# Performance work log

Hardware: AMD Instinct MI355X
Metric: run time of the kernel (lower is better)

## Reference

```python
import jax, jax.numpy as jnp
import numpy as np

B, S, E, H = 2, 2048, 1024, 16
D = E // H  # head_dim
SCALE = 1.0 / np.sqrt(D)


def rope_tables(seq_len, dim, dtype=jnp.float32):
    # matches RotaryEmbedding: inv_freq over even indices, emb = cat([freqs, freqs])
    inv_freq = 1.0 / (10000.0 ** (jnp.arange(0, dim, 2, dtype=dtype) / dim))
    t = jnp.arange(seq_len, dtype=dtype)
    freqs = t[:, None] * inv_freq[None, :]          # [S, D/2]
    emb = jnp.concatenate([freqs, freqs], axis=-1)  # [S, D]
    return jnp.cos(emb)[None, None], jnp.sin(emb)[None, None]  # [1,1,S,D]


def apply_rope(x, cos, sin):
    # x: [B,H,S,D]; interleaved rotate exactly as the torch code:
    # x2 = stack([-x[...,1::2], x[...,0::2]], -1).reshape_as(x)
    x2 = jnp.stack([-x[..., 1::2], x[..., 0::2]], axis=-1).reshape(x.shape)
    return x * cos + x2 * sin


def setup_inputs() -> dict:
    key = jax.random.key(0)
    ks = jax.random.split(key, 12)
    std = 1.0 / np.sqrt(E)
    inp = {
        "query": jax.random.normal(ks[0], (B, S, E), jnp.float32),
        "key": jax.random.normal(ks[1], (B, S, E), jnp.float32),
        "value": jax.random.normal(ks[2], (B, S, E), jnp.float32),
        "mask": jnp.ones((B, S), jnp.int32),
        "Wq": jax.random.normal(ks[3], (E, E), jnp.float32) * std,
        "bq": jax.random.normal(ks[4], (E,), jnp.float32) * std,
        "Wk": jax.random.normal(ks[5], (E, E), jnp.float32) * std,
        "bk": jax.random.normal(ks[6], (E,), jnp.float32) * std,
        "Wv": jax.random.normal(ks[7], (E, E), jnp.float32) * std,
        "bv": jax.random.normal(ks[8], (E,), jnp.float32) * std,
        "Wo": jax.random.normal(ks[9], (E, E), jnp.float32) * std,
        "bo": jax.random.normal(ks[10], (E,), jnp.float32) * std,
    }
    return inp


def reference(query, key, value, mask, Wq, bq, Wk, bk, Wv, bv, Wo, bo):
    b, sq, _ = query.shape
    sk = key.shape[1]
    # linear projections (torch Linear: x @ W.T + b), split into heads [B,H,S,D]
    Q = (query @ Wq.T + bq).reshape(b, sq, H, D).transpose(0, 2, 1, 3)
    K = (key @ Wk.T + bk).reshape(b, sk, H, D).transpose(0, 2, 1, 3)
    V = (value @ Wv.T + bv).reshape(b, sk, H, D).transpose(0, 2, 1, 3)
    cos_q, sin_q = rope_tables(sq, D)
    cos_k, sin_k = rope_tables(sk, D)
    Q = apply_rope(Q, cos_q, sin_q)
    K = apply_rope(K, cos_k, sin_k)
    scores = jnp.einsum("bhqd,bhkd->bhqk", Q, K) * SCALE
    neg_inf = jnp.finfo(scores.dtype).min
    scores = jnp.where(mask[:, None, None, :] == 0, neg_inf, scores)
    attn = jax.nn.softmax(scores, axis=-1)
    # dropout omitted (deterministic reference / eval mode)
    out = jnp.einsum("bhqk,bhkd->bhqd", attn, V)
    out = out.transpose(0, 2, 1, 3).reshape(b, sq, E)
    return out @ Wo.T + bo
```

## Files before the change

### kernel.cpp

```cpp
#include <hip/hip_runtime.h>
#include <stdint.h>

typedef unsigned short u16;
typedef __bf16 bf16x8 __attribute__((ext_vector_type(8)));
typedef float f32x4 __attribute__((ext_vector_type(4)));
typedef float f32x2 __attribute__((ext_vector_type(2)));
typedef u16 u16x4v __attribute__((ext_vector_type(4)));

#define DI __device__ __forceinline__

constexpr int BB = 2, SS = 2048, EE = 1024, HH = 16, DD = 64;
constexpr int MROWS = BB * SS;
constexpr int KDIM = 1024, NDIM = 1024;

constexpr float FM = 12.0f;
constexpr float MNEG = -30000.f;

DI u16 f2bf(float f) {
  uint32_t u = __float_as_uint(f);
  return (u16)((u + 0x7FFFu + ((u >> 16) & 1u)) >> 16);
}
DI float bf2f(u16 h) { return __uint_as_float(((uint32_t)h) << 16); }

DI uint32_t cvtpk_bf16(float a, float b) {
  uint32_t r;
  asm("v_cvt_pk_bf16_f32 %0, %1, %2" : "=v"(r) : "v"(a), "v"(b));
  return r;
}

DI void cp16(const void* g, void* lds) {
  __builtin_amdgcn_global_load_lds((const __attribute__((address_space(1))) void*)g,
                                   (__attribute__((address_space(3))) void*)lds, 16, 0, 0);
}

DI f32x4 mfma16(bf16x8 a, bf16x8 b, f32x4 c) {
  return __builtin_amdgcn_mfma_f32_16x16x32_bf16(a, b, c, 0, 0, 0);
}

__global__ __launch_bounds__(256) void prep_cast(
    const float* __restrict__ q, const float* __restrict__ k, const float* __restrict__ v,
    const float* __restrict__ wq, const float* __restrict__ wk, const float* __restrict__ wv,
    const float* __restrict__ wo,
    u16* __restrict__ qb, u16* __restrict__ kb, u16* __restrict__ vb,
    u16* __restrict__ wqb, u16* __restrict__ wkb, u16* __restrict__ wvb,
    u16* __restrict__ wob) {
  constexpr size_t SZI = (size_t)MROWS * EE;
  constexpr size_t SZW = (size_t)EE * EE;
  const size_t g = ((size_t)blockIdx.x * 256 + threadIdx.x) * 4;
  const float* src; u16* dst; size_t o;
  if (g < SZI)          { src = q; dst = qb; o = g; }
  else if (g < 2 * SZI) { src = k; dst = kb; o = g - SZI; }
  else if (g < 3 * SZI) { src = v; dst = vb; o = g - 2 * SZI; }
  else {
    size_t t2 = g - 3 * SZI;
    int wi = (int)(t2 / SZW);
    o = t2 - (size_t)(wi < 4 ? wi : 3) * SZW;
    src = wi == 0 ? wq : wi == 1 ? wk : wi == 2 ? wv : wo;
    dst = wi == 0 ? wqb : wi == 1 ? wkb : wi == 2 ? wvb : wob;
  }
  const float4 f = *(const float4*)(src + o);
  u16x4v hv;
  hv[0] = f2bf(f.x); hv[1] = f2bf(f.y); hv[2] = f2bf(f.z); hv[3] = f2bf(f.w);
  *(u16x4v*)(dst + o) = hv;
}

__global__ __launch_bounds__(256) void rope_tables_k(float* __restrict__ csT,
                                                     const int* __restrict__ mask,
                                                     float* __restrict__ mfl) {
  const int t = blockIdx.x * 256 + threadIdx.x;
  const int s = t >> 6, d = t & 63, j = d & 31;
  const float ang = (float)s * exp2f(-(float)j * 0.4152410118f);
  float2 cs; cs.x = cosf(ang); cs.y = sinf(ang);
  ((float2*)csT)[t] = cs;
  if (t < BB * SS) mfl[t] = mask[t] ? -FM : MNEG;
}

__global__ __launch_bounds__(256) void gemm_qkv(
    const u16* __restrict__ qb, const u16* __restrict__ kb, const u16* __restrict__ vb,
    const u16* __restrict__ wqb, const u16* __restrict__ wkb, const u16* __restrict__ wvb,
    const float* __restrict__ bq, const float* __restrict__ bk, const float* __restrict__ bv,
    u16* __restrict__ Qp, u16* __restrict__ Kp, u16* __restrict__ Vtg,
    const float* __restrict__ csT) {
  __shared__ alignas(16) u16 sA[2][128 * 64];
  __shared__ alignas(16) u16 sB[2][128 * 64];
  const int tsel = blockIdx.y >> 5;
  const bool vtr = (tsel == 2);
  const u16* A    = tsel == 0 ? wqb : tsel == 1 ? wkb : vb;
  const u16* Bm   = tsel == 0 ? qb  : tsel == 1 ? kb  : wvb;
  const float* bias = tsel == 0 ? bq : tsel == 1 ? bk : bv;

  const int fBase = blockIdx.x * 128;
  const int tBase = (blockIdx.y & 31) * 128;
  const int aBase = vtr ? tBase : fBase;
  const int bBase = vtr ? fBase : tBase;
  const int tid = threadIdx.x;
  const int lane = tid & 63, w = tid >> 6;
  const int quad = lane >> 4, l16 = lane & 15;
  const int wr = w >> 1, wc = w & 1;

  size_t aSrc[4], bSrc[4];
  int dOff[4];
#pragma unroll
  for (int j = 0; j < 4; ++j) {
    const int c = tid + j * 256;
    const int row = c >> 3, sl = c & 7;
    const size_t off = (size_t)row * KDIM + ((sl ^ (row & 7)) * 8);
    aSrc[j] = (size_t)aBase * KDIM + off;
    bSrc[j] = (size_t)bBase * KDIM + off;
    dOff[j] = c * 8;
  }

  f32x4 acc[4][4];
#pragma unroll
  for (int mi = 0; mi < 4; ++mi)
#pragma unroll
    for (int ni = 0; ni < 4; ++ni)
#pragma unroll
      for (int e = 0; e < 4; ++e) acc[mi][ni][e] = 0.f;

  const int arow = wr * 64 + l16, brow = wc * 64 + l16;

  auto stage = [&](int k0, int bi) {
#pragma unroll
    for (int j = 0; j < 4; ++j) {
      cp16(A + aSrc[j] + k0, &sA[bi][dOff[j]]);
      cp16(Bm + bSrc[j] + k0, &sB[bi][dOff[j]]);
    }
  };

  stage(0, 0);
  __syncthreads();
  int buf = 0;
  for (int k0 = 0; k0 < KDIM; k0 += 64) {
    if (k0 + 64 < KDIM) stage(k0 + 64, buf ^ 1);
    __builtin_amdgcn_s_setprio(1);
#pragma unroll
    for (int h = 0; h < 2; ++h) {
      bf16x8 af[4], bf[4];
#pragma unroll
      for (int i = 0; i < 4; ++i) {
        const int ar = arow + i * 16, br = brow + i * 16;
        af[i] = *(const bf16x8*)&sA[buf][ar * 64 + (((h * 4 + quad) ^ (ar & 7)) << 3)];
        bf[i] = *(const bf16x8*)&sB[buf][br * 64 + (((h * 4 + quad) ^ (br & 7)) << 3)];
      }
#pragma unroll
      for (int mi = 0; mi < 4; ++mi)
#pragma unroll
        for (int ni = 0; ni < 4; ++ni)
          acc[mi][ni] = mfma16(af[mi], bf[ni], acc[mi][ni]);
    }
    __builtin_amdgcn_s_setprio(0);
    __syncthreads();
    buf ^= 1;
  }

  if (!vtr) {
    u16* C = tsel == 0 ? Qp : Kp;
#pragma unroll
    for (int mi = 0; mi < 4; ++mi) {
      const int fm = fBase + wr * 64 + mi * 16 + quad * 4;
      const float4 b4 = *(const float4*)&bias[fm];
      const int d0 = fm & 63;
#pragma unroll
      for (int ni = 0; ni < 4; ++ni) {
        const int t = tBase + wc * 64 + ni * 16 + l16;
        const int srow = t & (SS - 1);
        const float* cs = &csT[(size_t)((srow << 6) + d0) * 2];
        const float4 cs01 = *(const float4*)cs;
        const float4 cs23 = *(const float4*)(cs + 4);
        const float v0 = acc[mi][ni][0] + b4.x;
        const float v1 = acc[mi][ni][1] + b4.y;
        const float v2 = acc[mi][ni][2] + b4.z;
        const float v3 = acc[mi][ni][3] + b4.w;
        const float o0 = v0 * cs01.x - v1 * cs01.y;
        const float o1 = v1 * cs01.z + v0 * cs01.w;
        const float o2 = v2 * cs23.x - v3 * cs23.y;
        const float o3 = v3 * cs23.z + v2 * cs23.w;
        uint2 pk;
        pk.x = cvtpk_bf16(o0, o1);
        pk.y = cvtpk_bf16(o2, o3);
        *(uint2*)&C[(size_t)t * NDIM + fm] = pk;
      }
    }
  } else {
#pragma unroll
    for (int ni = 0; ni < 4; ++ni) {
      const int f = fBase + wc * 64 + ni * 16 + l16;
      const int h = f >> 6, d = f & 63;
      const float bb = bias[f];
#pragma unroll
      for (int mi = 0; mi < 4; ++mi) {
        const int t0 = tBase + wr * 64 + mi * 16 + quad * 4;
        const int b = t0 >> 11, s0 = t0 & (SS - 1);
        const int sp0 = (s0 & ~31) | (((s0 >> 2) & 3) << 3) | (((s0 >> 4) & 1) << 2);
        uint2 pk;
        pk.x = cvtpk_bf16(acc[mi][ni][0] + bb, acc[mi][ni][1] + bb);
        pk.y = cvtpk_bf16(acc[mi][ni][2] + bb, acc[mi][ni][3] + bb);
        *(uint2*)&Vtg[((size_t)((b * 16 + h) * 64 + d)) * SS + sp0] = pk;
      }
    }
  }
}

__global__ __launch_bounds__(256, 2) void attn_kernel(
    const u16* __restrict__ Qp, const u16* __restrict__ Kp, const u16* __restrict__ Vtg,
    const float* __restrict__ mfl, u16* __restrict__ Oh) {
  __shared__ alignas(16) u16 sK[2][128 * 64];
  __shared__ alignas(16) u16 sVt[2][64 * 128];
  __shared__ alignas(16) float sMaskAll[SS];
  const int tid = threadIdx.x, lane = tid & 63, w = tid >> 6;
  const int quad = lane >> 4, l16 = lane & 15;
  const int bh = blockIdx.y, b = bh >> 4, h = bh & 15;
  const int q0 = blockIdx.x * 128 + w * 32;
  const u16* Qb = Qp + (size_t)b * SS * EE + h * DD;
  const u16* Kb = Kp + (size_t)b * SS * EE + h * DD;
  const u16* Vb = Vtg + (size_t)bh * DD * SS;
  constexpr float C1 = 0.18033688011112042f;

  bf16x8 qf[2][2];
#pragma unroll
  for (int qi = 0; qi < 2; ++qi)
#pragma unroll
    for (int ks = 0; ks < 2; ++ks)
      qf[qi][ks] = *(const bf16x8*)(Qb + (size_t)(q0 + qi * 16 + l16) * EE + ks * 32 + quad * 8);

  f32x4 oacc[2][4];
#pragma unroll
  for (int qi = 0; qi < 2; ++qi)
#pragma unroll
    for (int nd = 0; nd < 4; ++nd)
#pragma unroll
      for (int e = 0; e < 4; ++e) oacc[qi][nd][e] = 0.f;
  f32x2 sum2[2];
  sum2[0] = {0.f, 0.f}; sum2[1] = {0.f, 0.f};

  auto stage = [&](int kt, int bi) {
    const int key0 = kt * 128;
#pragma unroll
    for (int i = 0; i < 4; ++i) {
      const int c = i * 256 + tid;
      const int key = c >> 3;
      const int g8 = ((c & 7) ^ (key & 7)) * 8;
      cp16(Kb + (size_t)(key0 + key) * EE + g8, &sK[bi][c * 8]);
    }
#pragma unroll
    for (int i = 0; i < 4; ++i) {
      const int L = i * 256 + tid;
      const int d = L >> 4;
      const int g8 = ((L & 15) ^ (d & 15)) * 8;
      cp16(Vb + (size_t)d * SS + key0 + g8, &sVt[bi][L * 8]);
    }
  };

  auto compute = [&](int kt, int bi) {
    const int key0 = kt * 128;
    f32x4 sacc[2][8];
#pragma unroll
    for (int qi = 0; qi < 2; ++qi)
#pragma unroll
      for (int ni = 0; ni < 8; ++ni)
#pragma unroll
        for (int e = 0; e < 4; ++e) sacc[qi][ni][e] = 0.f;
    __builtin_amdgcn_s_setprio(1);
#pragma unroll
    for (int ks = 0; ks < 2; ++ks)
#pragma unroll
      for (int ni = 0; ni < 8; ++ni) {
        const int row = ni * 16 + l16;
        const bf16x8 kf = *(const bf16x8*)&sK[bi][row * 64 + (((ks * 4 + quad) ^ (l16 & 7)) << 3)];
#pragma unroll
        for (int qi = 0; qi < 2; ++qi)
          sacc[qi][ni] = mfma16(kf, qf[qi][ks], sacc[qi][ni]);
      }
    __builtin_amdgcn_s_setprio(0);

    uint32_t pw32[2][4][4];
#pragma unroll
    for (int qi = 0; qi < 2; ++qi)
#pragma unroll
      for (int ni = 0; ni < 8; ++ni) {
        const int kb4 = key0 + ni * 16 + quad * 4;
        const f32x2 m01 = *(const f32x2*)&sMaskAll[kb4];
        const f32x2 m23 = *(const f32x2*)&sMaskAll[kb4 + 2];
        f32x2 t01, t23;
        t01.x = sacc[qi][ni][0]; t01.y = sacc[qi][ni][1];
        t23.x = sacc[qi][ni][2]; t23.y = sacc[qi][ni][3];
        t01 = t01 * C1 + m01;
        t23 = t23 * C1 + m23;
        f32x2 p01, p23;
        p01.x = __builtin_amdgcn_exp2f(t01.x); p01.y = __builtin_amdgcn_exp2f(t01.y);
        p23.x = __builtin_amdgcn_exp2f(t23.x); p23.y = __builtin_amdgcn_exp2f(t23.y);
        sum2[qi] += p01;
        sum2[qi] += p23;
        const int k2 = ni >> 1, j2 = (ni & 1) * 2;
        pw32[qi][k2][j2]     = cvtpk_bf16(p01.x, p01.y);
        pw32[qi][k2][j2 + 1] = cvtpk_bf16(p23.x, p23.y);
      }

    __builtin_amdgcn_s_setprio(1);
#pragma unroll
    for (int k2 = 0; k2 < 4; ++k2) {
      union { uint32_t u[4]; bf16x8 v; } pf[2];
#pragma unroll
      for (int qi = 0; qi < 2; ++qi)
#pragma unroll
        for (int j = 0; j < 4; ++j) pf[qi].u[j] = pw32[qi][k2][j];
#pragma unroll
      for (int nd = 0; nd < 4; ++nd) {
        const int row = nd * 16 + l16;
        const bf16x8 vf = *(const bf16x8*)&sVt[bi][row * 128 + (((k2 * 4 + quad) ^ l16) << 3)];
#pragma unroll
        for (int qi = 0; qi < 2; ++qi)
          oacc[qi][nd] = mfma16(pf[qi].v, vf, oacc[qi][nd]);
      }
    }
    __builtin_amdgcn_s_setprio(0);
  };

  stage(0, 0);
#pragma unroll
  for (int i = 0; i < 2; ++i) {
    const int t4 = (i * 256 + tid) * 4;
    cp16(mfl + (size_t)b * SS + t4, &sMaskAll[t4]);
  }
  __syncthreads();

  for (int kt = 0; kt < SS / 128; kt += 2) {
    if (kt + 1 < SS / 128) stage(kt + 1, 1);
    compute(kt, 0);
    __syncthreads();
    if (kt + 2 < SS / 128) stage(kt + 2, 0);
    compute(kt + 1, 1);
    __syncthreads();
  }

  float linv[2];
#pragma unroll
  for (int qi = 0; qi < 2; ++qi) {
    float lrow = sum2[qi].x + sum2[qi].y;
    lrow += __shfl_xor(lrow, 16, 64);
    lrow += __shfl_xor(lrow, 32, 64);
    linv[qi] = lrow > 0.f ? 1.0f / lrow : 0.f;
  }

#pragma unroll
  for (int qi = 0; qi < 2; ++qi)
#pragma unroll
    for (int r = 0; r < 4; ++r) {
      const float li = __shfl(linv[qi], quad * 4 + r, 16);
      const size_t row = (size_t)(b * SS + q0 + qi * 16 + quad * 4 + r) * EE + h * DD;
#pragma unroll
      for (int nd = 0; nd < 4; ++nd) {
        const int d = nd * 16 + l16;
        Oh[row + d] = f2bf(oacc[qi][nd][r] * li);
      }
    }
}

__global__ __launch_bounds__(256) void gemm_out(
    const u16* __restrict__ Ab, const u16* __restrict__ Bb,
    const float* __restrict__ bias, float* __restrict__ Cout) {
  __shared__ alignas(16) u16 sA[2][128 * 64];
  __shared__ alignas(16) u16 sB[2][64 * 64];
  const int rowBase = blockIdx.y * 128;
  const int colBase = blockIdx.x * 64;
  const int tid = threadIdx.x;
  const int lane = tid & 63, w = tid >> 6;
  const int quad = lane >> 4, l16 = lane & 15;
  const int wr = w >> 1, wc = w & 1;

  size_t aSrc[4]; int aOff[4];
  size_t bSrc[2]; int bOff[2];
#pragma unroll
  for (int j = 0; j < 4; ++j) {
    const int c = tid + j * 256;
    const int row = c >> 3, sl = c & 7;
    aSrc[j] = (size_t)(rowBase + row) * KDIM + ((sl ^ (row & 7)) * 8);
    aOff[j] = c * 8;
  }
#pragma unroll
  for (int j = 0; j < 2; ++j) {
    const int c = tid + j * 256;
    const int row = c >> 3, sl = c & 7;
    bSrc[j] = (size_t)(colBase + row) * KDIM + ((sl ^ (row & 7)) * 8);
    bOff[j] = c * 8;
  }

  f32x4 acc[4][2];
#pragma unroll
  for (int mi = 0; mi < 4; ++mi)
#pragma unroll
    for (int ni = 0; ni < 2; ++ni)
#pragma unroll
      for (int e = 0; e < 4; ++e) acc[mi][ni][e] = 0.f;

  const int arow = wr * 64 + l16, brow = wc * 32 + l16;

  auto stage = [&](int k0, int bi) {
#pragma unroll
    for (int j = 0; j < 4; ++j) cp16(Ab + aSrc[j] + k0, &sA[bi][aOff[j]]);
#pragma unroll
    for (int j = 0; j < 2; ++j) cp16(Bb + bSrc[j] + k0, &sB[bi][bOff[j]]);
  };

  stage(0, 0);
  __syncthreads();
  int buf = 0;
  for (int k0 = 0; k0 < KDIM; k0 += 64) {
    if (k0 + 64 < KDIM) stage(k0 + 64, buf ^ 1);
    __builtin_amdgcn_s_setprio(1);
#pragma unroll
    for (int h = 0; h < 2; ++h) {
      bf16x8 af[4], bf[2];
#pragma unroll
      for (int i = 0; i < 4; ++i) {
        const int ar = arow + i * 16;
        af[i] = *(const bf16x8*)&sA[buf][ar * 64 + (((h * 4 + quad) ^ (ar & 7)) << 3)];
      }
#pragma unroll
      for (int i = 0; i < 2; ++i) {
        const int br = brow + i * 16;
        bf[i] = *(const bf16x8*)&sB[buf][br * 64 + (((h * 4 + quad) ^ (br & 7)) << 3)];
      }
#pragma unroll
      for (int mi = 0; mi < 4; ++mi)
#pragma unroll
        for (int ni = 0; ni < 2; ++ni)
          acc[mi][ni] = mfma16(af[mi], bf[ni], acc[mi][ni]);
    }
    __builtin_amdgcn_s_setprio(0);
    __syncthreads();
    buf ^= 1;
  }

#pragma unroll
  for (int mi = 0; mi < 4; ++mi) {
    const int rb = rowBase + wr * 64 + mi * 16 + quad * 4;
#pragma unroll
    for (int ni = 0; ni < 2; ++ni) {
      const int col = colBase + wc * 32 + ni * 16 + l16;
      const float bb = bias[col];
#pragma unroll
      for (int r = 0; r < 4; ++r)
        Cout[(size_t)(rb + r) * NDIM + col] = acc[mi][ni][r] + bb;
    }
  }
}

extern "C" void kernel_launch(void* const* d_in, const int* in_sizes, int n_in,
                              void* d_out, int out_size, void* d_ws, size_t ws_size,
                              hipStream_t stream) {
  const float* q    = (const float*)d_in[0];
  const float* k    = (const float*)d_in[1];
  const float* v    = (const float*)d_in[2];
  const int*   mask = (const int*)d_in[3];
  const float* Wq = (const float*)d_in[4];
  const float* bq = (const float*)d_in[5];
  const float* Wk = (const float*)d_in[6];
  const float* bk = (const float*)d_in[7];
  const float* Wv = (const float*)d_in[8];
  const float* bv = (const float*)d_in[9];
  const float* Wo = (const float*)d_in[10];
  const float* bo = (const float*)d_in[11];
  float* out = (float*)d_out;
  char* ws = (char*)d_ws;
  constexpr size_t MB = 1024 * 1024;
  u16* qb  = (u16*)(ws + 0 * MB);
  u16* kb  = (u16*)(ws + 8 * MB);
  u16* vb  = (u16*)(ws + 16 * MB);
  u16* wqb = (u16*)(ws + 24 * MB);
  u16* wkb = (u16*)(ws + 26 * MB);
  u16* wvb = (u16*)(ws + 28 * MB);
  u16* wob = (u16*)(ws + 30 * MB);
  u16* Qp  = (u16*)(ws + 32 * MB);
  u16* Kp  = (u16*)(ws + 40 * MB);
  u16* Vtg = (u16*)(ws + 48 * MB);
  u16* oh  = (u16*)(ws + 56 * MB);
  float* csT = (float*)(ws + 64 * MB);
  float* mfl = out;

  prep_cast<<<16384, 256, 0, stream>>>(q, k, v, Wq, Wk, Wv, Wo,
                                       qb, kb, vb, wqb, wkb, wvb, wob);
  rope_tables_k<<<512, 256, 0, stream>>>(csT, mask, mfl);
  gemm_qkv<<<dim3(8, 96), 256, 0, stream>>>(qb, kb, vb, wqb, wkb, wvb,
                                            bq, bk, bv, Qp, Kp, Vtg, csT);
  attn_kernel<<<dim3(16, 32), 256, 0, stream>>>(Qp, Kp, Vtg, mfl, oh);
  gemm_out<<<dim3(16, 32), 256, 0, stream>>>(oh, wob, bo, out);
}
```

Baseline: 231.1 us.

## Split attention key range across two wave groups with shared-memory merge

```diff
diff --git a/kernel.cpp b/kernel.cpp
--- a/kernel.cpp
+++ b/kernel.cpp
@@ -202,20 +202,20 @@
   }
 }
 
-__global__ __launch_bounds__(256, 2) void attn_kernel(
+__global__ __launch_bounds__(512, 4) void attn_kernel(
     const u16* __restrict__ Qp, const u16* __restrict__ Kp, const u16* __restrict__ Vtg,
     const float* __restrict__ mfl, u16* __restrict__ Oh) {
-  __shared__ alignas(16) u16 sK[2][128 * 64];
-  __shared__ alignas(16) u16 sVt[2][64 * 128];
-  __shared__ alignas(16) float sMaskAll[SS];
+  __shared__ alignas(16) u16 sm[36864];
   const int tid = threadIdx.x, lane = tid & 63, w = tid >> 6;
   const int quad = lane >> 4, l16 = lane & 15;
+  const int grp = w >> 2, wl = w & 3;
   const int bh = blockIdx.y, b = bh >> 4, h = bh & 15;
-  const int q0 = blockIdx.x * 128 + w * 32;
+  const int q0 = blockIdx.x * 128 + wl * 32;
   const u16* Qb = Qp + (size_t)b * SS * EE + h * DD;
   const u16* Kb = Kp + (size_t)b * SS * EE + h * DD;
   const u16* Vb = Vtg + (size_t)bh * DD * SS;
   constexpr float C1 = 0.18033688011112042f;
+  float* smask = (float*)&sm[32768];
 
   bf16x8 qf[2][2];
 #pragma unroll
@@ -234,54 +234,58 @@
   f32x2 sum2[2];
   sum2[0] = {0.f, 0.f}; sum2[1] = {0.f, 0.f};
 
-  auto stage = [&](int kt, int bi) {
-    const int key0 = kt * 128;
-#pragma unroll
-    for (int i = 0; i < 4; ++i) {
-      const int c = i * 256 + tid;
-      const int key = c >> 3;
-      const int g8 = ((c & 7) ^ (key & 7)) * 8;
-      cp16(Kb + (size_t)(key0 + key) * EE + g8, &sK[bi][c * 8]);
-    }
-#pragma unroll
-    for (int i = 0; i < 4; ++i) {
-      const int L = i * 256 + tid;
-      const int d = L >> 4;
-      const int g8 = ((L & 15) ^ (d & 15)) * 8;
-      cp16(Vb + (size_t)d * SS + key0 + g8, &sVt[bi][L * 8]);
+  const int gtid = tid & 255;
+
+  auto stage = [&](int w_, int bi) {
+    const int key0 = w_ * 128 + grp * 64;
+    u16* dK = &sm[grp * 16384 + bi * 4096];
+    u16* dV = &sm[grp * 16384 + 8192 + bi * 4096];
+#pragma unroll
+    for (int i = 0; i < 2; ++i) {
+      const int c = i * 256 + gtid;
+      const int key = c >> 3, sl = c & 7;
+      cp16(Kb + (size_t)(key0 + key) * EE + ((sl ^ (key & 7)) * 8), &dK[c * 8]);
+    }
+#pragma unroll
+    for (int i = 0; i < 2; ++i) {
+      const int c = i * 256 + gtid;
+      const int d = c >> 3, sl = c & 7;
+      cp16(Vb + (size_t)d * SS + key0 + ((sl ^ (d & 7)) * 8), &dV[c * 8]);
     }
   };
 
-  auto compute = [&](int kt, int bi) {
-    const int key0 = kt * 128;
-    f32x4 sacc[2][8];
+  auto compute = [&](int w_, int bi) {
+    const int key0 = w_ * 128 + grp * 64;
+    const u16* sK_ = &sm[grp * 16384 + bi * 4096];
+    const u16* sV_ = &sm[grp * 16384 + 8192 + bi * 4096];
+    f32x4 sacc[2][4];
 #pragma unroll
     for (int qi = 0; qi < 2; ++qi)
 #pragma unroll
-      for (int ni = 0; ni < 8; ++ni)
+      for (int ni = 0; ni < 4; ++ni)
 #pragma unroll
         for (int e = 0; e < 4; ++e) sacc[qi][ni][e] = 0.f;
     __builtin_amdgcn_s_setprio(1);
 #pragma unroll
     for (int ks = 0; ks < 2; ++ks)
 #pragma unroll
-      for (int ni = 0; ni < 8; ++ni) {
+      for (int ni = 0; ni < 4; ++ni) {
         const int row = ni * 16 + l16;
-        const bf16x8 kf = *(const bf16x8*)&sK[bi][row * 64 + (((ks * 4 + quad) ^ (l16 & 7)) << 3)];
+        const bf16x8 kf = *(const bf16x8*)&sK_[row * 64 + (((ks * 4 + quad) ^ (l16 & 7)) << 3)];
 #pragma unroll
         for (int qi = 0; qi < 2; ++qi)
           sacc[qi][ni] = mfma16(kf, qf[qi][ks], sacc[qi][ni]);
       }
     __builtin_amdgcn_s_setprio(0);
 
-    uint32_t pw32[2][4][4];
+    uint32_t pw32[2][2][4];
 #pragma unroll
     for (int qi = 0; qi < 2; ++qi)
 #pragma unroll
-      for (int ni = 0; ni < 8; ++ni) {
+      for (int ni = 0; ni < 4; ++ni) {
         const int kb4 = key0 + ni * 16 + quad * 4;
-        const f32x2 m01 = *(const f32x2*)&sMaskAll[kb4];
-        const f32x2 m23 = *(const f32x2*)&sMaskAll[kb4 + 2];
+        const f32x2 m01 = *(const f32x2*)&smask[kb4];
+        const f32x2 m23 = *(const f32x2*)&smask[kb4 + 2];
         f32x2 t01, t23;
         t01.x = sacc[qi][ni][0]; t01.y = sacc[qi][ni][1];
         t23.x = sacc[qi][ni][2]; t23.y = sacc[qi][ni][3];
@@ -299,7 +303,7 @@
 
     __builtin_amdgcn_s_setprio(1);
 #pragma unroll
-    for (int k2 = 0; k2 < 4; ++k2) {
+    for (int k2 = 0; k2 < 2; ++k2) {
       union { uint32_t u[4]; bf16x8 v; } pf[2];
 #pragma unroll
       for (int qi = 0; qi < 2; ++qi)
@@ -308,7 +312,7 @@
 #pragma unroll
       for (int nd = 0; nd < 4; ++nd) {
         const int row = nd * 16 + l16;
-        const bf16x8 vf = *(const bf16x8*)&sVt[bi][row * 128 + (((k2 * 4 + quad) ^ l16) << 3)];
+        const bf16x8 vf = *(const bf16x8*)&sV_[row * 64 + (((k2 * 4 + quad) ^ (l16 & 7)) << 3)];
 #pragma unroll
         for (int qi = 0; qi < 2; ++qi)
           oacc[qi][nd] = mfma16(pf[qi].v, vf, oacc[qi][nd]);
@@ -318,43 +322,63 @@
   };
 
   stage(0, 0);
-#pragma unroll
-  for (int i = 0; i < 2; ++i) {
-    const int t4 = (i * 256 + tid) * 4;
-    cp16(mfl + (size_t)b * SS + t4, &sMaskAll[t4]);
-  }
+  cp16(mfl + (size_t)b * SS + tid * 4, &sm[32768 + tid * 8]);
   __syncthreads();
 
-  for (int kt = 0; kt < SS / 128; kt += 2) {
-    if (kt + 1 < SS / 128) stage(kt + 1, 1);
-    compute(kt, 0);
+  for (int w_ = 0; w_ < 16; ++w_) {
+    if (w_ + 1 < 16) stage(w_ + 1, (w_ + 1) & 1);
+    compute(w_, w_ & 1);
     __syncthreads();
-    if (kt + 2 < SS / 128) stage(kt + 2, 0);
-    compute(kt + 1, 1);
-    __syncthreads();
-  }
-
-  float linv[2];
+  }
+
+  float lg[2];
 #pragma unroll
   for (int qi = 0; qi < 2; ++qi) {
-    float lrow = sum2[qi].x + sum2[qi].y;
-    lrow += __shfl_xor(lrow, 16, 64);
-    lrow += __shfl_xor(lrow, 32, 64);
-    linv[qi] = lrow > 0.f ? 1.0f / lrow : 0.f;
-  }
-
-#pragma unroll
-  for (int qi = 0; qi < 2; ++qi)
-#pragma unroll
-    for (int r = 0; r < 4; ++r) {
-      const float li = __shfl(linv[qi], quad * 4 + r, 16);
-      const size_t row = (size_t)(b * SS + q0 + qi * 16 + quad * 4 + r) * EE + h * DD;
-#pragma unroll
-      for (int nd = 0; nd < 4; ++nd) {
-        const int d = nd * 16 + l16;
-        Oh[row + d] = f2bf(oacc[qi][nd][r] * li);
-      }
-    }
+    float s = sum2[qi].x + sum2[qi].y;
+    s += __shfl_xor(s, 16, 64);
+    s += __shfl_xor(s, 32, 64);
+    lg[qi] = s;
+  }
+
+  float* sO = (float*)&sm[0];
+  float* l0 = smask;
+  if (grp == 0) {
+#pragma unroll
+    for (int qi = 0; qi < 2; ++qi)
+#pragma unroll
+      for (int nd = 0; nd < 4; ++nd)
+#pragma unroll
+        for (int e = 0; e < 4; ++e) {
+          const int q = wl * 32 + qi * 16 + quad * 4 + e;
+          sO[q * 65 + nd * 16 + l16] = oacc[qi][nd][e];
+        }
+    if (quad == 0) {
+      l0[wl * 32 + l16] = lg[0];
+      l0[wl * 32 + 16 + l16] = lg[1];
+    }
+  }
+  __syncthreads();
+  if (grp == 1) {
+    float linv[2];
+#pragma unroll
+    for (int qi = 0; qi < 2; ++qi) {
+      const float lt = l0[wl * 32 + qi * 16 + l16] + lg[qi];
+      linv[qi] = lt > 0.f ? 1.0f / lt : 0.f;
+    }
+#pragma unroll
+    for (int qi = 0; qi < 2; ++qi)
+#pragma unroll
+      for (int r = 0; r < 4; ++r) {
+        const float li = __shfl(linv[qi], quad * 4 + r, 16);
+        const int q = wl * 32 + qi * 16 + quad * 4 + r;
+        const size_t row = (size_t)(b * SS + blockIdx.x * 128 + q) * EE + h * DD;
+#pragma unroll
+        for (int nd = 0; nd < 4; ++nd) {
+          const int d = nd * 16 + l16;
+          Oh[row + d] = f2bf((sO[q * 65 + d] + oacc[qi][nd][r]) * li);
+        }
+      }
+  }
 }
 
 __global__ __launch_bounds__(256) void gemm_out(
@@ -484,6 +508,6 @@
   rope_tables_k<<<512, 256, 0, stream>>>(csT, mask, mfl);
   gemm_qkv<<<dim3(8, 96), 256, 0, stream>>>(qb, kb, vb, wqb, wkb, wvb,
                                             bq, bk, bv, Qp, Kp, Vtg, csT);
-  attn_kernel<<<dim3(16, 32), 256, 0, stream>>>(Qp, Kp, Vtg, mfl, oh);
+  attn_kernel<<<dim3(16, 32), 512, 0, stream>>>(Qp, Kp, Vtg, mfl, oh);
   gemm_out<<<dim3(16, 32), 256, 0, stream>>>(oh, wob, bo, out);
 }
```

Result: faster. 223.0 us (-3.5%).
